# Kernel optimization log

Hardware: AMD Instinct MI355X
Metric: run time of the kernel (lower is better)

## Reference

```python
import jax, jax.numpy as jnp
import numpy as np

NUM_HEADS = 8
HEAD_DIM = 64
WIN = (8, 8, 8)  # (wT, wH, wW)


def setup_inputs() -> dict:
    key = jax.random.key(0)
    k1, k2, k3 = jax.random.split(key, 3)
    B, T, H, W, C = 2, 16, 32, 32, 512
    d_inner = NUM_HEADS * HEAD_DIM  # 512
    x = jax.random.normal(k1, (B, T * H * W, C), dtype=jnp.float32)
    # torch Linear weights stored transposed as [in, out] for y = x @ w
    w_qkv = jax.random.normal(k2, (C, 3 * d_inner), dtype=jnp.float32) * (C ** -0.5)
    w_proj = jax.random.normal(k3, (d_inner, C), dtype=jnp.float32) * (d_inner ** -0.5)
    b_proj = jnp.zeros((C,), dtype=jnp.float32)
    return {"x": x, "w_qkv": w_qkv, "w_proj": w_proj, "b_proj": b_proj,
            "T": T, "H": H, "W": W}


def reference(x, w_qkv, w_proj, b_proj, T, H, W):
    B, N, C = x.shape
    wT, wH, wW = WIN
    scale = HEAD_DIM ** -0.5
    # module re-derives T if N mismatches T*H*W
    if N != T * H * W:
        T = N // (H * W)
    xv = x.reshape(B, T, H, W, C)
    pt, ph, pw = (-T) % wT, (-H) % wH, (-W) % wW
    if pt or ph or pw:
        xv = jnp.pad(xv, ((0, 0), (0, pt), (0, ph), (0, pw), (0, 0)))
    Tp, Hp, Wp = T + pt, H + ph, W + pw
    nT, nH, nW = Tp // wT, Hp // wH, Wp // wW
    L = wT * wH * wW  # tokens per window
    # window partition: [B*nT*nH*nW, L, C]
    xw = xv.reshape(B, nT, wT, nH, wH, nW, wW, C)
    xw = xw.transpose(0, 1, 3, 5, 2, 4, 6, 7).reshape(-1, L, C)
    # qkv projection (no bias)
    qkv = xw @ w_qkv  # [nw, L, 3*nh*hd]
    q, k, v = jnp.split(qkv, 3, axis=-1)

    def heads(t):
        return t.reshape(t.shape[0], L, NUM_HEADS, HEAD_DIM).transpose(0, 2, 1, 3)

    q, k, v = heads(q), heads(k), heads(v)  # [nw, h, L, d]
    attn = jax.nn.softmax(jnp.einsum('nhid,nhjd->nhij', q, k) * scale, axis=-1)
    o = jnp.einsum('nhij,nhjd->nhid', attn, v)
    o = o.transpose(0, 2, 1, 3).reshape(-1, L, NUM_HEADS * HEAD_DIM)
    o = o @ w_proj + b_proj  # output projection
    # window un-partition
    o = o.reshape(B, nT, nH, nW, wT, wH, wW, C)
    o = o.transpose(0, 1, 4, 2, 5, 3, 6, 7).reshape(B, Tp, Hp, Wp, C)
    return o[:, :T, :H, :W].reshape(B, N, C)
```

## Files before the change

kernel.cpp:

```cpp
#include <hip/hip_runtime.h>
#include <hip/hip_bf16.h>

typedef __hip_bfloat16 bf16;
typedef __attribute__((ext_vector_type(8))) short bf16x8;
typedef __attribute__((ext_vector_type(4))) float f32x4;

#define MROWS 32768
#define CDIM 512
#define SEL_STRIDE (512*512*64)

__device__ __forceinline__ int win_to_src_row(int m) {
  int win = m >> 9, l = m & 511;
  int b = win >> 5, rr = win & 31;
  int nt = rr >> 4, nh = (rr >> 2) & 3, nw = rr & 3;
  int wt = l >> 6, wh = (l >> 3) & 7, ww = l & 7;
  int tt = nt * 8 + wt, hh = nh * 8 + wh, wp = nw * 8 + ww;
  return (b << 14) + (tt << 10) + (hh << 5) + wp;
}

__global__ __launch_bounds__(256) void transpose_cvt_kernel(
    const float* __restrict__ src, bf16* __restrict__ dst, int R, int C) {
  __shared__ float tile[32][33];
  int bc = blockIdx.x * 32, br = blockIdx.y * 32;
  int tx = threadIdx.x, ty = threadIdx.y;
#pragma unroll
  for (int i = 0; i < 32; i += 8)
    tile[ty + i][tx] = src[(size_t)(br + ty + i) * C + bc + tx];
  __syncthreads();
#pragma unroll
  for (int i = 0; i < 32; i += 8)
    dst[(size_t)(bc + ty + i) * R + br + tx] = __float2bfloat16(tile[tx][ty + i]);
}

__global__ __launch_bounds__(256) void perm_x_kernel(const float* __restrict__ x,
                                                     bf16* __restrict__ xw) {
  int m = blockIdx.x;
  int src = win_to_src_row(m);
  const float* s = x + (size_t)src * CDIM;
  bf16* d = xw + (size_t)m * CDIM;
  int c = threadIdx.x * 2;
  float2 v = *(const float2*)(s + c);
  __hip_bfloat162 o;
  o.x = __float2bfloat16(v.x);
  o.y = __float2bfloat16(v.y);
  *(__hip_bfloat162*)(d + c) = o;
}

#define BM 128
#define BN 128
#define BK 64

__device__ __forceinline__ void gload16(const bf16* g, bf16* l) {
  __builtin_amdgcn_global_load_lds(
      (const __attribute__((address_space(1))) unsigned int*)g,
      (__attribute__((address_space(3))) unsigned int*)l, 16, 0, 0);
}

template <int MODE>
__global__ __launch_bounds__(256) void gemm_bt_kernel(
    const bf16* __restrict__ A, const bf16* __restrict__ Bt, int Mtiles,
    bf16* __restrict__ qkv_out, float* __restrict__ out,
    const float* __restrict__ bias) {
  __shared__ __align__(16) bf16 Asl[BM * BK];
  __shared__ __align__(16) bf16 Bsl[BN * BK];
  const int K = 512;
  int bx = blockIdx.x;
  int bm = bx % Mtiles, bn = bx / Mtiles;
  int t = threadIdx.x, lane = t & 63, w = t >> 6;
  int wr = w >> 1, wc = w & 1;
  int l15 = lane & 15, lh = lane >> 4;
  f32x4 acc[4][4] = {};

  for (int kt = 0; kt < K; kt += BK) {
    __syncthreads();
#pragma unroll
    for (int i = 0; i < 4; ++i) {
      int f = i * 256 + t;
      int row = f >> 3, cb = f & 7;
      gload16(A + (size_t)(bm * BM + row) * K + kt + cb * 8,
              &Asl[(i * 256 + w * 64) * 8]);
    }
#pragma unroll
    for (int i = 0; i < 4; ++i) {
      int f = i * 256 + t;
      int row = f >> 3, cb = f & 7;
      gload16(Bt + (size_t)(bn * BN + row) * K + kt + cb * 8,
              &Bsl[(i * 256 + w * 64) * 8]);
    }
    __syncthreads();
#pragma unroll
    for (int kk = 0; kk < 2; ++kk) {
      bf16x8 af[4], bfr[4];
#pragma unroll
      for (int mi = 0; mi < 4; ++mi)
        af[mi] = *(const bf16x8*)&Asl[(wr * 64 + mi * 16 + l15) * BK + kk * 32 + lh * 8];
#pragma unroll
      for (int nj = 0; nj < 4; ++nj)
        bfr[nj] = *(const bf16x8*)&Bsl[(wc * 64 + nj * 16 + l15) * BK + kk * 32 + lh * 8];
#pragma unroll
      for (int mi = 0; mi < 4; ++mi)
#pragma unroll
        for (int nj = 0; nj < 4; ++nj)
          acc[mi][nj] = __builtin_amdgcn_mfma_f32_16x16x32_bf16(
              af[mi], bfr[nj], acc[mi][nj], 0, 0, 0);
    }
  }

  if (MODE == 0) {
#pragma unroll
    for (int mi = 0; mi < 4; ++mi) {
      int row = bm * BM + wr * 64 + mi * 16 + lh * 4;
      int win = row >> 9, tok = row & 511;
#pragma unroll
      for (int nj = 0; nj < 4; ++nj) {
        int col = bn * BN + wc * 64 + nj * 16 + l15;
        int sel = col >> 9, cc = col & 511;
        int head = cc >> 6, d = cc & 63;
        size_t base = (size_t)sel * SEL_STRIDE +
                      (((size_t)(win * 8 + head)) * 512 + tok) * 64 + d;
#pragma unroll
        for (int r = 0; r < 4; ++r)
          qkv_out[base + (size_t)r * 64] = __float2bfloat16(acc[mi][nj][r]);
      }
    }
  } else {
#pragma unroll
    for (int mi = 0; mi < 4; ++mi) {
      int row = bm * BM + wr * 64 + mi * 16 + lh * 4;
#pragma unroll
      for (int r = 0; r < 4; ++r) {
        int srow = win_to_src_row(row + r);
        float* op = out + (size_t)srow * CDIM;
#pragma unroll
        for (int nj = 0; nj < 4; ++nj) {
          int col = bn * BN + wc * 64 + nj * 16 + l15;
          op[col] = acc[mi][nj][r] + bias[col];
        }
      }
    }
  }
}

__global__ __launch_bounds__(256) void attn_kernel(const bf16* __restrict__ qkv_ws,
                                                   bf16* __restrict__ o_ws) {
  __shared__ __align__(16) bf16 Kl[512 * 64];
  __shared__ __align__(16) bf16 Vl[64 * 512];
  __shared__ __align__(16) bf16 Pl[4][16 * 64];
  int wh = blockIdx.x;
  int win = wh >> 3, head = wh & 7;
  int t = threadIdx.x, lane = t & 63, w = t >> 6;
  int l15 = lane & 15, lh = lane >> 4;
  const bf16* qb = qkv_ws + (size_t)wh * (512 * 64);
  const bf16* kb = qb + SEL_STRIDE;
  const bf16* vb = qb + 2 * (size_t)SEL_STRIDE;

  for (int i = 0; i < 16; ++i) {
    int f = i * 256 + t;
    int row = f >> 3, cb = (f & 7) << 4;
    uint4 v = *(const uint4*)((const char*)kb + row * 128 + cb);
    *(uint4*)((char*)Kl + row * 128 + (cb ^ ((row & 7) << 4))) = v;
  }
  for (int i = 0; i < 16; ++i) {
    int f = i * 256 + t;
    int tok = f >> 3, d0 = (f & 7) * 8;
    uint4 v = *(const uint4*)((const char*)vb + tok * 128 + d0 * 2);
    const bf16* pv = (const bf16*)&v;
#pragma unroll
    for (int j = 0; j < 8; ++j) {
      int d = d0 + j;
      *(bf16*)((char*)Vl + d * 1024 + ((tok * 2) ^ ((d & 7) << 4))) = pv[j];
    }
  }
  __syncthreads();

  const float scale = 0.125f;
  for (int qc = 0; qc < 4; ++qc) {
    int q0 = qc * 128 + w * 32;
    bf16x8 qf[2][2];
#pragma unroll
    for (int qi = 0; qi < 2; ++qi)
#pragma unroll
      for (int kk = 0; kk < 2; ++kk)
        qf[qi][kk] = *(const bf16x8*)(qb + (size_t)(q0 + qi * 16 + l15) * 64 + kk * 32 + lh * 8);
    f32x4 acco[2][4] = {};
    float lsum[2][4] = {};
    for (int kt = 0; kt < 8; ++kt) {
      bf16x8 kf[4][2], vf[4][2];
#pragma unroll
      for (int kj = 0; kj < 4; ++kj) {
        int tok = kt * 64 + kj * 16 + l15;
#pragma unroll
        for (int kk = 0; kk < 2; ++kk)
          kf[kj][kk] = *(const bf16x8*)((const char*)Kl + tok * 128 +
                                        ((kk * 64 + lh * 16) ^ ((tok & 7) << 4)));
      }
#pragma unroll
      for (int nj = 0; nj < 4; ++nj) {
        int d = nj * 16 + l15;
#pragma unroll
        for (int kk = 0; kk < 2; ++kk)
          vf[nj][kk] = *(const bf16x8*)((const char*)Vl + d * 1024 +
                                        (((kt * 64 + kk * 32 + lh * 8) * 2) ^ ((d & 7) << 4)));
      }
#pragma unroll
      for (int qi = 0; qi < 2; ++qi) {
        f32x4 s[4] = {};
#pragma unroll
        for (int kj = 0; kj < 4; ++kj)
#pragma unroll
          for (int kk = 0; kk < 2; ++kk)
            s[kj] = __builtin_amdgcn_mfma_f32_16x16x32_bf16(qf[qi][kk], kf[kj][kk], s[kj], 0, 0, 0);
        float rs[4] = {0.f, 0.f, 0.f, 0.f};
#pragma unroll
        for (int kj = 0; kj < 4; ++kj)
#pragma unroll
          for (int r = 0; r < 4; ++r) {
            float p = __expf(s[kj][r] * scale);
            s[kj][r] = p;
            rs[r] += p;
          }
#pragma unroll
        for (int r = 0; r < 4; ++r) {
          float v = rs[r];
          v += __shfl_xor(v, 1);
          v += __shfl_xor(v, 2);
          v += __shfl_xor(v, 4);
          v += __shfl_xor(v, 8);
          lsum[qi][r] += v;
        }
#pragma unroll
        for (int kj = 0; kj < 4; ++kj)
#pragma unroll
          for (int r = 0; r < 4; ++r) {
            int prow = lh * 4 + r, pcol = kj * 16 + l15;
            *(bf16*)((char*)&Pl[w][0] + prow * 128 + ((pcol * 2) ^ ((prow & 7) << 4))) =
                __float2bfloat16(s[kj][r]);
          }
        bf16x8 pa[2];
#pragma unroll
        for (int kk = 0; kk < 2; ++kk)
          pa[kk] = *(const bf16x8*)((const char*)&Pl[w][0] + l15 * 128 +
                                    ((kk * 64 + lh * 16) ^ ((l15 & 7) << 4)));
#pragma unroll
        for (int nj = 0; nj < 4; ++nj)
#pragma unroll
          for (int kk = 0; kk < 2; ++kk)
            acco[qi][nj] = __builtin_amdgcn_mfma_f32_16x16x32_bf16(pa[kk], vf[nj][kk],
                                                                   acco[qi][nj], 0, 0, 0);
      }
    }
#pragma unroll
    for (int qi = 0; qi < 2; ++qi)
#pragma unroll
      for (int nj = 0; nj < 4; ++nj)
#pragma unroll
        for (int r = 0; r < 4; ++r) {
          int row = q0 + qi * 16 + lh * 4 + r;
          int d = nj * 16 + l15;
          float v = acco[qi][nj][r] / lsum[qi][r];
          o_ws[((size_t)win * 512 + row) * 512 + head * 64 + d] = __float2bfloat16(v);
        }
  }
}

extern "C" void kernel_launch(void* const* d_in, const int* in_sizes, int n_in,
                              void* d_out, int out_size, void* d_ws, size_t ws_size,
                              hipStream_t stream) {
  const float* x = (const float*)d_in[0];
  const float* w_qkv = (const float*)d_in[1];
  const float* w_proj = (const float*)d_in[2];
  const float* b_proj = (const float*)d_in[3];
  float* out = (float*)d_out;

  const size_t OFF_QKV = 33554432;
  const size_t OFF_WQ = OFF_QKV + 100663296;
  const size_t OFF_WP = OFF_WQ + 1572864;
  const size_t NEED = OFF_WP + 524288;
  if (ws_size < NEED) return;

  char* ws = (char*)d_ws;
  bf16* xw = (bf16*)ws;
  bf16* qkv = (bf16*)(ws + OFF_QKV);
  bf16* wqkvT = (bf16*)(ws + OFF_WQ);
  bf16* wprojT = (bf16*)(ws + OFF_WP);
  bf16* o_ws = xw;

  transpose_cvt_kernel<<<dim3(1536 / 32, 512 / 32), dim3(32, 8), 0, stream>>>(w_qkv, wqkvT, 512, 1536);
  transpose_cvt_kernel<<<dim3(512 / 32, 512 / 32), dim3(32, 8), 0, stream>>>(w_proj, wprojT, 512, 512);
  perm_x_kernel<<<MROWS, 256, 0, stream>>>(x, xw);
  gemm_bt_kernel<0><<<256 * 12, 256, 0, stream>>>(xw, wqkvT, 256, qkv, nullptr, nullptr);
  attn_kernel<<<512, 256, 0, stream>>>(qkv, o_ws);
  gemm_bt_kernel<1><<<256 * 4, 256, 0, stream>>>(o_ws, wprojT, 256, nullptr, out, b_proj);
}
```

Baseline: 255.6 us.

## Split attention across query chunks, pre-transpose V, XCD-aware block swizzle

The attention kernel now launches one block per (window, head, query chunk), 2048 blocks instead of 512. It drops the LDS staging of K and V and reads K and a pre-transposed V straight from global memory. The QKV GEMM epilogue writes V in transposed layout with packed 4-element stores, and both GEMMs and the attention kernel remap block indices so neighbouring tiles run on the same XCD for L2 reuse. The permute kernel becomes a grid-stride loop with float4 loads, and the final normalisation multiplies by a reciprocal instead of dividing. The aim is better occupancy and less LDS and sync overhead in attention, at the cost of K and V being read from global or L2 once per query chunk.

```diff
diff --git a/kernel.cpp b/kernel.cpp
--- a/kernel.cpp
+++ b/kernel.cpp
@@ -18,6 +18,14 @@
   return (b << 14) + (tt << 10) + (hh << 5) + wp;
 }
 
+__device__ __forceinline__ unsigned short bf16bits(bf16 h) {
+  return __builtin_bit_cast(unsigned short, h);
+}
+
+__device__ __forceinline__ int xcd_chunk(int bx, int n) {
+  return (bx & 7) * (n >> 3) + (bx >> 3);
+}
+
 __global__ __launch_bounds__(256) void transpose_cvt_kernel(
     const float* __restrict__ src, bf16* __restrict__ dst, int R, int C) {
   __shared__ float tile[32][33];
@@ -34,16 +42,18 @@
 
 __global__ __launch_bounds__(256) void perm_x_kernel(const float* __restrict__ x,
                                                      bf16* __restrict__ xw) {
-  int m = blockIdx.x;
-  int src = win_to_src_row(m);
-  const float* s = x + (size_t)src * CDIM;
-  bf16* d = xw + (size_t)m * CDIM;
-  int c = threadIdx.x * 2;
-  float2 v = *(const float2*)(s + c);
-  __hip_bfloat162 o;
-  o.x = __float2bfloat16(v.x);
-  o.y = __float2bfloat16(v.y);
-  *(__hip_bfloat162*)(d + c) = o;
+  const int total = MROWS * (CDIM / 4);
+  for (int i = blockIdx.x * 256 + threadIdx.x; i < total; i += 2048 * 256) {
+    int m = i >> 7, c4 = (i & 127) * 4;
+    int src = win_to_src_row(m);
+    float4 v = *(const float4*)(x + (size_t)src * CDIM + c4);
+    ushort4 o;
+    o.x = bf16bits(__float2bfloat16(v.x));
+    o.y = bf16bits(__float2bfloat16(v.y));
+    o.z = bf16bits(__float2bfloat16(v.z));
+    o.w = bf16bits(__float2bfloat16(v.w));
+    *(ushort4*)(xw + (size_t)m * CDIM + c4) = o;
+  }
 }
 
 #define BM 128
@@ -58,14 +68,15 @@
 
 template <int MODE>
 __global__ __launch_bounds__(256) void gemm_bt_kernel(
-    const bf16* __restrict__ A, const bf16* __restrict__ Bt, int Mtiles,
+    const bf16* __restrict__ A, const bf16* __restrict__ Bt, int Ntiles,
     bf16* __restrict__ qkv_out, float* __restrict__ out,
     const float* __restrict__ bias) {
   __shared__ __align__(16) bf16 Asl[BM * BK];
   __shared__ __align__(16) bf16 Bsl[BN * BK];
   const int K = 512;
-  int bx = blockIdx.x;
-  int bm = bx % Mtiles, bn = bx / Mtiles;
+  int l2 = xcd_chunk(blockIdx.x, gridDim.x);
+  int bn = (l2 >> 3) % Ntiles;
+  int bm = (l2 & 7) + (l2 / (8 * Ntiles)) * 8;
   int t = threadIdx.x, lane = t & 63, w = t >> 6;
   int wr = w >> 1, wc = w & 1;
   int l15 = lane & 15, lh = lane >> 4;
@@ -116,11 +127,21 @@
         int col = bn * BN + wc * 64 + nj * 16 + l15;
         int sel = col >> 9, cc = col & 511;
         int head = cc >> 6, d = cc & 63;
-        size_t base = (size_t)sel * SEL_STRIDE +
-                      (((size_t)(win * 8 + head)) * 512 + tok) * 64 + d;
-#pragma unroll
-        for (int r = 0; r < 4; ++r)
-          qkv_out[base + (size_t)r * 64] = __float2bfloat16(acc[mi][nj][r]);
+        if (sel == 2) {
+          ushort4 pk;
+          pk.x = bf16bits(__float2bfloat16(acc[mi][nj][0]));
+          pk.y = bf16bits(__float2bfloat16(acc[mi][nj][1]));
+          pk.z = bf16bits(__float2bfloat16(acc[mi][nj][2]));
+          pk.w = bf16bits(__float2bfloat16(acc[mi][nj][3]));
+          *(ushort4*)(qkv_out + 2 * (size_t)SEL_STRIDE +
+                      (((size_t)(win * 8 + head)) * 64 + d) * 512 + tok) = pk;
+        } else {
+          size_t base = (size_t)sel * SEL_STRIDE +
+                        (((size_t)(win * 8 + head)) * 512 + tok) * 64 + d;
+#pragma unroll
+          for (int r = 0; r < 4; ++r)
+            qkv_out[base + (size_t)r * 64] = __float2bfloat16(acc[mi][nj][r]);
+        }
       }
     }
   } else {
@@ -143,123 +164,104 @@
 
 __global__ __launch_bounds__(256) void attn_kernel(const bf16* __restrict__ qkv_ws,
                                                    bf16* __restrict__ o_ws) {
-  __shared__ __align__(16) bf16 Kl[512 * 64];
-  __shared__ __align__(16) bf16 Vl[64 * 512];
   __shared__ __align__(16) bf16 Pl[4][16 * 64];
-  int wh = blockIdx.x;
+  int l2 = xcd_chunk(blockIdx.x, 2048);
+  int wh = l2 >> 2, qc = l2 & 3;
   int win = wh >> 3, head = wh & 7;
   int t = threadIdx.x, lane = t & 63, w = t >> 6;
   int l15 = lane & 15, lh = lane >> 4;
   const bf16* qb = qkv_ws + (size_t)wh * (512 * 64);
   const bf16* kb = qb + SEL_STRIDE;
-  const bf16* vb = qb + 2 * (size_t)SEL_STRIDE;
-
-  for (int i = 0; i < 16; ++i) {
-    int f = i * 256 + t;
-    int row = f >> 3, cb = (f & 7) << 4;
-    uint4 v = *(const uint4*)((const char*)kb + row * 128 + cb);
-    *(uint4*)((char*)Kl + row * 128 + (cb ^ ((row & 7) << 4))) = v;
-  }
-  for (int i = 0; i < 16; ++i) {
-    int f = i * 256 + t;
-    int tok = f >> 3, d0 = (f & 7) * 8;
-    uint4 v = *(const uint4*)((const char*)vb + tok * 128 + d0 * 2);
-    const bf16* pv = (const bf16*)&v;
-#pragma unroll
-    for (int j = 0; j < 8; ++j) {
-      int d = d0 + j;
-      *(bf16*)((char*)Vl + d * 1024 + ((tok * 2) ^ ((d & 7) << 4))) = pv[j];
-    }
-  }
-  __syncthreads();
+  const bf16* vtb = qkv_ws + 2 * (size_t)SEL_STRIDE + (size_t)wh * (64 * 512);
 
   const float scale = 0.125f;
-  for (int qc = 0; qc < 4; ++qc) {
-    int q0 = qc * 128 + w * 32;
-    bf16x8 qf[2][2];
-#pragma unroll
-    for (int qi = 0; qi < 2; ++qi)
+  int q0 = qc * 128 + w * 32;
+  bf16x8 qf[2][2];
+#pragma unroll
+  for (int qi = 0; qi < 2; ++qi)
+#pragma unroll
+    for (int kk = 0; kk < 2; ++kk)
+      qf[qi][kk] = *(const bf16x8*)(qb + (size_t)(q0 + qi * 16 + l15) * 64 + kk * 32 + lh * 8);
+
+  f32x4 acco[2][4] = {};
+  float lsum[2][4] = {};
+  for (int kt = 0; kt < 8; ++kt) {
+    bf16x8 kf[4][2], vf[4][2];
+#pragma unroll
+    for (int kj = 0; kj < 4; ++kj) {
+      int tok = kt * 64 + kj * 16 + l15;
 #pragma unroll
       for (int kk = 0; kk < 2; ++kk)
-        qf[qi][kk] = *(const bf16x8*)(qb + (size_t)(q0 + qi * 16 + l15) * 64 + kk * 32 + lh * 8);
-    f32x4 acco[2][4] = {};
-    float lsum[2][4] = {};
-    for (int kt = 0; kt < 8; ++kt) {
-      bf16x8 kf[4][2], vf[4][2];
-#pragma unroll
-      for (int kj = 0; kj < 4; ++kj) {
-        int tok = kt * 64 + kj * 16 + l15;
+        kf[kj][kk] = *(const bf16x8*)(kb + (size_t)tok * 64 + kk * 32 + lh * 8);
+    }
+#pragma unroll
+    for (int nj = 0; nj < 4; ++nj) {
+      int d = nj * 16 + l15;
+#pragma unroll
+      for (int kk = 0; kk < 2; ++kk)
+        vf[nj][kk] = *(const bf16x8*)(vtb + (size_t)d * 512 + kt * 64 + kk * 32 + lh * 8);
+    }
+#pragma unroll
+    for (int qi = 0; qi < 2; ++qi) {
+      f32x4 s[4] = {};
+#pragma unroll
+      for (int kj = 0; kj < 4; ++kj)
 #pragma unroll
         for (int kk = 0; kk < 2; ++kk)
-          kf[kj][kk] = *(const bf16x8*)((const char*)Kl + tok * 128 +
-                                        ((kk * 64 + lh * 16) ^ ((tok & 7) << 4)));
-      }
-#pragma unroll
-      for (int nj = 0; nj < 4; ++nj) {
+          s[kj] = __builtin_amdgcn_mfma_f32_16x16x32_bf16(qf[qi][kk], kf[kj][kk], s[kj], 0, 0, 0);
+      float rs[4] = {0.f, 0.f, 0.f, 0.f};
+#pragma unroll
+      for (int kj = 0; kj < 4; ++kj)
+#pragma unroll
+        for (int r = 0; r < 4; ++r) {
+          float p = __expf(s[kj][r] * scale);
+          s[kj][r] = p;
+          rs[r] += p;
+        }
+#pragma unroll
+      for (int r = 0; r < 4; ++r) {
+        float v = rs[r];
+        v += __shfl_xor(v, 1);
+        v += __shfl_xor(v, 2);
+        v += __shfl_xor(v, 4);
+        v += __shfl_xor(v, 8);
+        lsum[qi][r] += v;
+      }
+#pragma unroll
+      for (int kj = 0; kj < 4; ++kj)
+#pragma unroll
+        for (int r = 0; r < 4; ++r) {
+          int prow = lh * 4 + r, pcol = kj * 16 + l15;
+          *(bf16*)((char*)&Pl[w][0] + prow * 128 + ((pcol * 2) ^ ((prow & 7) << 4))) =
+              __float2bfloat16(s[kj][r]);
+        }
+      bf16x8 pa[2];
+#pragma unroll
+      for (int kk = 0; kk < 2; ++kk)
+        pa[kk] = *(const bf16x8*)((const char*)&Pl[w][0] + l15 * 128 +
+                                  ((kk * 64 + lh * 16) ^ ((l15 & 7) << 4)));
+#pragma unroll
+      for (int nj = 0; nj < 4; ++nj)
+#pragma unroll
+        for (int kk = 0; kk < 2; ++kk)
+          acco[qi][nj] = __builtin_amdgcn_mfma_f32_16x16x32_bf16(pa[kk], vf[nj][kk],
+                                                                 acco[qi][nj], 0, 0, 0);
+    }
+  }
+#pragma unroll
+  for (int qi = 0; qi < 2; ++qi) {
+    float inv[4];
+#pragma unroll
+    for (int r = 0; r < 4; ++r) inv[r] = __frcp_rn(lsum[qi][r]);
+#pragma unroll
+    for (int nj = 0; nj < 4; ++nj)
+#pragma unroll
+      for (int r = 0; r < 4; ++r) {
+        int row = q0 + qi * 16 + lh * 4 + r;
         int d = nj * 16 + l15;
-#pragma unroll
-        for (int kk = 0; kk < 2; ++kk)
-          vf[nj][kk] = *(const bf16x8*)((const char*)Vl + d * 1024 +
-                                        (((kt * 64 + kk * 32 + lh * 8) * 2) ^ ((d & 7) << 4)));
-      }
-#pragma unroll
-      for (int qi = 0; qi < 2; ++qi) {
-        f32x4 s[4] = {};
-#pragma unroll
-        for (int kj = 0; kj < 4; ++kj)
-#pragma unroll
-          for (int kk = 0; kk < 2; ++kk)
-            s[kj] = __builtin_amdgcn_mfma_f32_16x16x32_bf16(qf[qi][kk], kf[kj][kk], s[kj], 0, 0, 0);
-        float rs[4] = {0.f, 0.f, 0.f, 0.f};
-#pragma unroll
-        for (int kj = 0; kj < 4; ++kj)
-#pragma unroll
-          for (int r = 0; r < 4; ++r) {
-            float p = __expf(s[kj][r] * scale);
-            s[kj][r] = p;
-            rs[r] += p;
-          }
-#pragma unroll
-        for (int r = 0; r < 4; ++r) {
-          float v = rs[r];
-          v += __shfl_xor(v, 1);
-          v += __shfl_xor(v, 2);
-          v += __shfl_xor(v, 4);
-          v += __shfl_xor(v, 8);
-          lsum[qi][r] += v;
-        }
-#pragma unroll
-        for (int kj = 0; kj < 4; ++kj)
-#pragma unroll
-          for (int r = 0; r < 4; ++r) {
-            int prow = lh * 4 + r, pcol = kj * 16 + l15;
-            *(bf16*)((char*)&Pl[w][0] + prow * 128 + ((pcol * 2) ^ ((prow & 7) << 4))) =
-                __float2bfloat16(s[kj][r]);
-          }
-        bf16x8 pa[2];
-#pragma unroll
-        for (int kk = 0; kk < 2; ++kk)
-          pa[kk] = *(const bf16x8*)((const char*)&Pl[w][0] + l15 * 128 +
-                                    ((kk * 64 + lh * 16) ^ ((l15 & 7) << 4)));
-#pragma unroll
-        for (int nj = 0; nj < 4; ++nj)
-#pragma unroll
-          for (int kk = 0; kk < 2; ++kk)
-            acco[qi][nj] = __builtin_amdgcn_mfma_f32_16x16x32_bf16(pa[kk], vf[nj][kk],
-                                                                   acco[qi][nj], 0, 0, 0);
-      }
-    }
-#pragma unroll
-    for (int qi = 0; qi < 2; ++qi)
-#pragma unroll
-      for (int nj = 0; nj < 4; ++nj)
-#pragma unroll
-        for (int r = 0; r < 4; ++r) {
-          int row = q0 + qi * 16 + lh * 4 + r;
-          int d = nj * 16 + l15;
-          float v = acco[qi][nj][r] / lsum[qi][r];
-          o_ws[((size_t)win * 512 + row) * 512 + head * 64 + d] = __float2bfloat16(v);
-        }
+        o_ws[((size_t)win * 512 + row) * 512 + head * 64 + d] =
+            __float2bfloat16(acco[qi][nj][r] * inv[r]);
+      }
   }
 }
 
@@ -287,8 +289,8 @@
 
   transpose_cvt_kernel<<<dim3(1536 / 32, 512 / 32), dim3(32, 8), 0, stream>>>(w_qkv, wqkvT, 512, 1536);
   transpose_cvt_kernel<<<dim3(512 / 32, 512 / 32), dim3(32, 8), 0, stream>>>(w_proj, wprojT, 512, 512);
-  perm_x_kernel<<<MROWS, 256, 0, stream>>>(x, xw);
-  gemm_bt_kernel<0><<<256 * 12, 256, 0, stream>>>(xw, wqkvT, 256, qkv, nullptr, nullptr);
-  attn_kernel<<<512, 256, 0, stream>>>(qkv, o_ws);
-  gemm_bt_kernel<1><<<256 * 4, 256, 0, stream>>>(o_ws, wprojT, 256, nullptr, out, b_proj);
-}
+  perm_x_kernel<<<2048, 256, 0, stream>>>(x, xw);
+  gemm_bt_kernel<0><<<256 * 12, 256, 0, stream>>>(xw, wqkvT, 12, qkv, nullptr, nullptr);
+  attn_kernel<<<2048, 256, 0, stream>>>(qkv, o_ws);
+  gemm_bt_kernel<1><<<256 * 4, 256, 0, stream>>>(o_ws, wprojT, 4, nullptr, out, b_proj);
+}
```

Measured after the change: 270.4 us. 1.06x slower.
